# Kernel optimization log

Measured on AMD Instinct MI355X. Metric: run time of the kernel, lower is better.

## Reference

```python
import jax, jax.numpy as jnp
import numpy as np

B, P, N, D = 128, 2048, 256, 2

def setup_inputs() -> dict:
    key = jax.random.key(0)
    k1, k2, k3 = jax.random.split(key, 3)
    batch = jax.random.normal(k1, (B, P, D), dtype=jnp.float32)
    not_dummy = jnp.ones((B, P), dtype=jnp.float32)
    centers = jax.random.uniform(k2, (N, D), dtype=jnp.float32)
    sharpness = jax.random.uniform(k3, (N, D), dtype=jnp.float32)
    exponent = jnp.ones((1,), dtype=jnp.float32)
    return {"batch": batch, "not_dummy": not_dummy, "centers": centers,
            "sharpness": sharpness, "exponent": exponent}

def reference(batch, not_dummy, centers, sharpness, exponent):
    # batch: (B, P, D); centers/sharpness: (N, D); exponent: (1,)
    # weighted L1 distance from each point to each structure element: (B, N, P)
    diff = jnp.abs(centers[None, :, None, :] - batch[:, None, :, :])
    s = jnp.sum(diff * jnp.abs(sharpness)[None, :, None, :], axis=-1)
    # rational kernel, mask out dummy (padding) points, sum-pool over points
    r = 1.0 / (1.0 + s ** exponent[0])
    r = r * not_dummy[:, None, :]
    return jnp.sum(r, axis=-1)  # (B, N)
```

## Files before the change

kernel.cpp:

```cpp
#include <hip/hip_runtime.h>

constexpr int B  = 128;
constexpr int P  = 2048;
constexpr int N  = 256;
constexpr int NT = 16;
constexpr int TPB = 256;
constexpr int PITER = P / TPB;

__global__ __launch_bounds__(TPB)
void SLayerRational_43190191128606_kernel(
    const float* __restrict__ batch,
    const float* __restrict__ not_dummy,
    const float* __restrict__ centers,
    const float* __restrict__ sharpness,
    const float* __restrict__ exponent,
    float* __restrict__ out)
{
    const int b   = blockIdx.x >> 4;
    const int n0  = (blockIdx.x & 15) * NT;
    const int tid = threadIdx.x;

    float c0[NT], c1[NT], a0[NT], a1[NT];
#pragma unroll
    for (int i = 0; i < NT; ++i) {
        c0[i] = centers[(n0 + i) * 2 + 0];
        c1[i] = centers[(n0 + i) * 2 + 1];
        a0[i] = fabsf(sharpness[(n0 + i) * 2 + 0]);
        a1[i] = fabsf(sharpness[(n0 + i) * 2 + 1]);
    }
    const float e = exponent[0];

    float acc[NT];
#pragma unroll
    for (int i = 0; i < NT; ++i) acc[i] = 0.0f;

    const float2* bb = reinterpret_cast<const float2*>(batch) + (size_t)b * P;
    const float*  nd = not_dummy + (size_t)b * P;

    if (e == 1.0f) {
#pragma unroll 2
        for (int k = 0; k < PITER; ++k) {
            const int p = tid + k * TPB;
            const float2 x = bb[p];
            const float  w = nd[p];
#pragma unroll
            for (int i = 0; i < NT; ++i) {
                float s = fmaf(fabsf(c0[i] - x.x), a0[i],
                               fabsf(c1[i] - x.y) * a1[i]);
                float r = __builtin_amdgcn_rcpf(1.0f + s);
                acc[i] = fmaf(w, r, acc[i]);
            }
        }
    } else {
        for (int k = 0; k < PITER; ++k) {
            const int p = tid + k * TPB;
            const float2 x = bb[p];
            const float  w = nd[p];
#pragma unroll
            for (int i = 0; i < NT; ++i) {
                float s = fmaf(fabsf(c0[i] - x.x), a0[i],
                               fabsf(c1[i] - x.y) * a1[i]);
                float r = w / (1.0f + powf(s, e));
                acc[i] += r;
            }
        }
    }

#pragma unroll
    for (int i = 0; i < NT; ++i) {
#pragma unroll
        for (int off = 32; off > 0; off >>= 1)
            acc[i] += __shfl_down(acc[i], off, 64);
    }

    __shared__ float red[4][NT];
    const int wave = tid >> 6;
    const int lane = tid & 63;
    if (lane == 0) {
#pragma unroll
        for (int i = 0; i < NT; ++i) red[wave][i] = acc[i];
    }
    __syncthreads();

    if (tid < NT) {
        float ssum = red[0][tid] + red[1][tid] + red[2][tid] + red[3][tid];
        out[b * N + n0 + tid] = ssum;
    }
}

extern "C" void kernel_launch(void* const* d_in, const int* in_sizes, int n_in,
                              void* d_out, int out_size, void* d_ws, size_t ws_size,
                              hipStream_t stream) {
    const float* batch     = (const float*)d_in[0];
    const float* not_dummy = (const float*)d_in[1];
    const float* centers   = (const float*)d_in[2];
    const float* sharpness = (const float*)d_in[3];
    const float* exponent  = (const float*)d_in[4];
    float* out = (float*)d_out;

    const int blocks = B * (N / NT);
    SLayerRational_43190191128606_kernel<<<blocks, TPB, 0, stream>>>(
        batch, not_dummy, centers, sharpness, exponent, out);
}
```

Before: 20.78 us.

## Pair points to share one reciprocal and split centers across waves

Each wave now handles 4 of the block's 16 centers and loops over all points of the batch row, which removes the shared-memory reduction and the block barrier. In the exponent==1 path, two points are combined as (wa*ub + wb*ua)/(ua*ub), so one reciprocal covers two terms and the transcendental work is halved. Center parameters are forced into scalar registers with readfirstlane, and launch bounds request higher occupancy. The trade-offs are that each wave now loads the whole point row (more load traffic per wave) and that the fused fraction can lose precision or overflow when the products grow large.

Result: slower. 21.21 us (+2.1%).

```diff
diff --git a/kernel.cpp b/kernel.cpp
--- a/kernel.cpp
+++ b/kernel.cpp
@@ -1,13 +1,19 @@
 #include <hip/hip_runtime.h>
 
-constexpr int B  = 128;
-constexpr int P  = 2048;
-constexpr int N  = 256;
-constexpr int NT = 16;
-constexpr int TPB = 256;
-constexpr int PITER = P / TPB;
+constexpr int B      = 128;
+constexpr int P      = 2048;
+constexpr int N      = 256;
+constexpr int TPB    = 256;
+constexpr int CPW    = 4;
+constexpr int NPB    = 16;
+constexpr int PITER  = P / 64;
+constexpr int GROUPS = PITER / 2;
 
-__global__ __launch_bounds__(TPB)
+__device__ __forceinline__ float rdfl(float v) {
+    return __int_as_float(__builtin_amdgcn_readfirstlane(__float_as_int(v)));
+}
+
+__global__ __launch_bounds__(TPB, 8)
 void SLayerRational_43190191128606_kernel(
     const float* __restrict__ batch,
     const float* __restrict__ not_dummy,
@@ -16,75 +22,79 @@
     const float* __restrict__ exponent,
     float* __restrict__ out)
 {
-    const int b   = blockIdx.x >> 4;
-    const int n0  = (blockIdx.x & 15) * NT;
-    const int tid = threadIdx.x;
+    const int b    = blockIdx.x >> 4;
+    const int n0   = (blockIdx.x & 15) * NPB;
+    const int wave = threadIdx.x >> 6;
+    const int lane = threadIdx.x & 63;
+    const int nw   = n0 + wave * CPW;
 
-    float c0[NT], c1[NT], a0[NT], a1[NT];
+    float c0[CPW], c1[CPW], a0[CPW], a1[CPW];
 #pragma unroll
-    for (int i = 0; i < NT; ++i) {
-        c0[i] = centers[(n0 + i) * 2 + 0];
-        c1[i] = centers[(n0 + i) * 2 + 1];
-        a0[i] = fabsf(sharpness[(n0 + i) * 2 + 0]);
-        a1[i] = fabsf(sharpness[(n0 + i) * 2 + 1]);
+    for (int c = 0; c < CPW; ++c) {
+        c0[c] = rdfl(centers[(nw + c) * 2 + 0]);
+        c1[c] = rdfl(centers[(nw + c) * 2 + 1]);
+        a0[c] = rdfl(fabsf(sharpness[(nw + c) * 2 + 0]));
+        a1[c] = rdfl(fabsf(sharpness[(nw + c) * 2 + 1]));
     }
     const float e = exponent[0];
 
-    float acc[NT];
+    float acc[CPW];
 #pragma unroll
-    for (int i = 0; i < NT; ++i) acc[i] = 0.0f;
+    for (int c = 0; c < CPW; ++c) acc[c] = 0.0f;
 
     const float2* bb = reinterpret_cast<const float2*>(batch) + (size_t)b * P;
     const float*  nd = not_dummy + (size_t)b * P;
 
     if (e == 1.0f) {
-#pragma unroll 2
-        for (int k = 0; k < PITER; ++k) {
-            const int p = tid + k * TPB;
+#pragma unroll 4
+        for (int g = 0; g < GROUPS; ++g) {
+            const int p = g * 128 + lane;
+            const float2 xa = bb[p];
+            const float2 xb = bb[p + 64];
+            const float  wa = nd[p];
+            const float  wb = nd[p + 64];
+#pragma unroll
+            for (int c = 0; c < CPW; ++c) {
+                const float d0a = c0[c] - xa.x;
+                const float d1a = c1[c] - xa.y;
+                const float ua  = fmaf(fabsf(d0a), a0[c],
+                                   fmaf(fabsf(d1a), a1[c], 1.0f));
+                const float d0b = c0[c] - xb.x;
+                const float d1b = c1[c] - xb.y;
+                const float ub  = fmaf(fabsf(d0b), a0[c],
+                                   fmaf(fabsf(d1b), a1[c], 1.0f));
+                float num = wa * ub;
+                num = fmaf(wb, ua, num);
+                const float den = ua * ub;
+                const float r   = __builtin_amdgcn_rcpf(den);
+                acc[c] = fmaf(num, r, acc[c]);
+            }
+        }
+    } else {
+        for (int it = 0; it < PITER; ++it) {
+            const int p = it * 64 + lane;
             const float2 x = bb[p];
             const float  w = nd[p];
 #pragma unroll
-            for (int i = 0; i < NT; ++i) {
-                float s = fmaf(fabsf(c0[i] - x.x), a0[i],
-                               fabsf(c1[i] - x.y) * a1[i]);
-                float r = __builtin_amdgcn_rcpf(1.0f + s);
-                acc[i] = fmaf(w, r, acc[i]);
-            }
-        }
-    } else {
-        for (int k = 0; k < PITER; ++k) {
-            const int p = tid + k * TPB;
-            const float2 x = bb[p];
-            const float  w = nd[p];
-#pragma unroll
-            for (int i = 0; i < NT; ++i) {
-                float s = fmaf(fabsf(c0[i] - x.x), a0[i],
-                               fabsf(c1[i] - x.y) * a1[i]);
-                float r = w / (1.0f + powf(s, e));
-                acc[i] += r;
+            for (int c = 0; c < CPW; ++c) {
+                const float s = fmaf(fabsf(c0[c] - x.x), a0[c],
+                                     fabsf(c1[c] - x.y) * a1[c]);
+                acc[c] += w / (1.0f + powf(s, e));
             }
         }
     }
 
 #pragma unroll
-    for (int i = 0; i < NT; ++i) {
+    for (int c = 0; c < CPW; ++c) {
 #pragma unroll
         for (int off = 32; off > 0; off >>= 1)
-            acc[i] += __shfl_down(acc[i], off, 64);
+            acc[c] += __shfl_down(acc[c], off, 64);
     }
 
-    __shared__ float red[4][NT];
-    const int wave = tid >> 6;
-    const int lane = tid & 63;
     if (lane == 0) {
 #pragma unroll
-        for (int i = 0; i < NT; ++i) red[wave][i] = acc[i];
-    }
-    __syncthreads();
-
-    if (tid < NT) {
-        float ssum = red[0][tid] + red[1][tid] + red[2][tid] + red[3][tid];
-        out[b * N + n0 + tid] = ssum;
+        for (int c = 0; c < CPW; ++c)
+            out[b * N + nw + c] = acc[c];
     }
 }
 
@@ -98,7 +108,7 @@
     const float* exponent  = (const float*)d_in[4];
     float* out = (float*)d_out;
 
-    const int blocks = B * (N / NT);
+    const int blocks = B * (N / NPB);
     SLayerRational_43190191128606_kernel<<<blocks, TPB, 0, stream>>>(
         batch, not_dummy, centers, sharpness, exponent, out);
 }
```
